# Optimization experiments

Measured on AMD Instinct MI355X. Metric: run time of the kernel, lower is better.

Reference implementation:

```python
import jax, jax.numpy as jnp
import numpy as np

EPS = 1e-5
C = 128
B = 16384
SYMBIOTIC = 4.0
NUM_PARENTS = 16
CHILDREN_PER_PARENT = 7


def _inverse(v):
    # torch: sort -> rank -> reversed rank -> gather sorted values
    idx0 = np.argsort(v, kind='stable')
    value = v[idx0]
    idx1 = np.argsort(idx0, kind='stable')  # ranks
    idx2 = v.shape[0] - 1 - idx1
    return value[idx2]


def _build_stats():
    counts = np.floor(50000.0 * 0.97 ** np.arange(C)) + 1.0  # long-tailed
    N = counts.sum()
    weight = (N / counts).astype(np.float32)
    prior = np.eye(C, dtype=np.float32)
    for p in range(NUM_PARENTS):
        ch = NUM_PARENTS + CHILDREN_PER_PARENT * p + np.arange(CHILDREN_PER_PARENT)
        prior[p, ch] = 1.0
    prior_me = (prior == 0).astype(np.float32)          # 1 - prior, keep only exact 1s
    prior_ms = prior - np.eye(C, dtype=np.float32)      # prior (0/1) minus eye
    v1_sig = np.log(N / counts - 1.0 + EPS).astype(np.float32)
    v2_sig = _inverse(v1_sig).astype(np.float32)
    v1_sm = np.log(counts / N + EPS).astype(np.float32)
    v2_sm = _inverse(v1_sm).astype(np.float32)
    return weight, prior_me, prior_ms, v1_sig, v2_sig, v1_sm, v2_sm


def setup_inputs() -> dict:
    key = jax.random.key(0)
    k1, k2 = jax.random.split(key)
    weight, prior_me, prior_ms, v1s, v2s, v1m, v2m = _build_stats()
    logits = 0.5 * jax.random.normal(k1, (12, B, C), dtype=jnp.float32)
    target = (jax.random.uniform(k2, (B, C)) < 0.1).astype(jnp.float32)
    return {
        'logits': logits, 'target': target,
        'weight': jnp.asarray(weight),
        'prior_me': jnp.asarray(prior_me), 'prior_ms': jnp.asarray(prior_ms),
        'v1_sigmoid': jnp.asarray(v1s), 'v2_sigmoid': jnp.asarray(v2s),
        'v1_softmax': jnp.asarray(v1m), 'v2_softmax': jnp.asarray(v2m),
    }


def reference(logits, target, weight, prior_me, prior_ms,
              v1_sigmoid, v2_sigmoid, v1_softmax, v2_softmax):
    zero = jnp.zeros_like(v1_sigmoid)
    # experts 0-5: sigmoid variants (long-tailed / balanced / inversed, twice)
    sig_shift = jnp.stack([zero, v1_sigmoid, v1_sigmoid - v2_sigmoid] * 2)  # [6,C]
    a_sig = jax.nn.sigmoid(logits[:6] - sig_shift[:, None, :])
    # experts 6-11: local-softmax variants
    sm_shift = jnp.stack([zero, v1_softmax, v1_softmax - v2_softmax] * 2)   # [6,C]
    e = jnp.exp(logits[6:] + sm_shift[:, None, :])                          # [6,B,C]
    denom = jnp.einsum('ebc,cd->ebd', e, prior_me) + e
    a_sm = e / (denom + EPS)
    acti = jnp.clip(jnp.concatenate([a_sig, a_sm], axis=0), EPS, 1.0 - EPS)  # [12,B,C]
    # weighted BCE per expert, summed
    bce = -weight * (target * jnp.log(acti) + (1.0 - target) * jnp.log(1.0 - acti))
    loss = jnp.sum(jnp.mean(bce, axis=(1, 2)))
    # symbiotic regularizer on experts 3,4,5,9,10,11
    row_sum = jnp.sum(prior_ms, axis=1)                 # [C]
    n_nz = jnp.sum(row_sum > 0).astype(acti.dtype)
    bsz = acti.shape[1]

    def symb(a):  # a: [B,C] activated logits
        def step(acc, xs):
            mask_row, parent = xs                       # [C], [B]
            term = jnp.log1p(jnp.exp(a - parent[:, None]))  # [B,C]
            rs = jnp.sum(mask_row)
            contrib = jnp.where(rs > 0, jnp.sum(term * mask_row) / (bsz * rs), 0.0)
            return acc + contrib, None
        total, _ = jax.lax.scan(step, jnp.float32(0.0), (prior_ms, a.T))
        return total / n_nz

    reg = jax.vmap(symb)(acti[jnp.array([3, 4, 5, 9, 10, 11])])
    return loss + SYMBIOTIC * jnp.sum(reg)
```

## Files before the change

### kernel.cpp

```cpp
#include <hip/hip_runtime.h>
#include <math.h>

#define CC 128
#define BB 16384
#define MEPS 1e-5f
#define NBLK 2048
#define PSZ ((size_t)BB * CC)


__device__ __forceinline__ float softplus1(float d) {
    const float u = d * d;
    float p = fmaf(u, 3.4722222e-4f, -5.2083333e-3f);
    p = fmaf(u, p, 0.125f);
    return fmaf(u, p, fmaf(d, 0.5f, 0.69314718f));
}

__global__ __launch_bounds__(256) void mel_main(
    const float* __restrict__ logits, const float* __restrict__ target,
    const float* __restrict__ weight,
    const float* __restrict__ v1s, const float* __restrict__ v2s,
    const float* __restrict__ v1m, const float* __restrict__ v2m,
    float* __restrict__ partial)
{
    const int lane = threadIdx.x & 63;
    const int wib  = threadIdx.x >> 6;
    const int wave = blockIdx.x * 4 + wib;
    const int r    = lane >> 5;
    const int c    = lane & 31;
    const size_t ro = (size_t)(wave * 2 + r) * CC;

    const float4 wt4 = ((const float4*)weight)[c];
    const float4 s1v = ((const float4*)v1s)[c];
    const float4 s2v = ((const float4*)v2s)[c];
    const float4 m1v = ((const float4*)v1m)[c];
    const float4 m2v = ((const float4*)v2m)[c];
    const float4 tv  = ((const float4*)(target + ro))[c];

    const float wt[4] = {wt4.x, wt4.y, wt4.z, wt4.w};
    const float s1[4] = {s1v.x, s1v.y, s1v.z, s1v.w};
    const float sd[4] = {s1v.x - s2v.x, s1v.y - s2v.y, s1v.z - s2v.z, s1v.w - s2v.w};
    const float m1[4] = {m1v.x, m1v.y, m1v.z, m1v.w};
    const float md[4] = {m1v.x - m2v.x, m1v.y - m2v.y, m1v.z - m2v.z, m1v.w - m2v.w};
    const bool  tb[4] = {tv.x > 0.5f, tv.y > 0.5f, tv.z > 0.5f, tv.w > 0.5f};

    const float childf = (c >= 4) ? 1.f : 0.f;
    int pofs[4];
    #pragma unroll
    for (int k = 0; k < 4; ++k) {
        const int ch = 4 * c + k;
        pofs[k] = (ch >= 16) ? (ch - 16) / 7 : 0;
    }

    __shared__ float lds[4][2][3][16];
    float* Lp = &lds[wib][r][0][0];

    const float* plane = logits + ro;
    float4 L0 = ((const float4*)plane)[c];
    float4 L1 = ((const float4*)(plane + PSZ))[c];
    float4 L2 = ((const float4*)(plane + 2 * PSZ))[c];
    plane += 3 * PSZ;

    float PnA[4] = {1.f, 1.f, 1.f, 1.f}, PdA[4] = {1.f, 1.f, 1.f, 1.f};
    float PnB[4] = {1.f, 1.f, 1.f, 1.f}, PdB[4] = {1.f, 1.f, 1.f, 1.f};
    float accS = 0.f;

    #pragma unroll 1
    for (int g = 0; g < 2; ++g) {
        const float x0[4] = {L0.x, L0.y, L0.z, L0.w};
        const float x1[4] = {L1.x, L1.y, L1.z, L1.w};
        const float x2[4] = {L2.x, L2.y, L2.z, L2.w};
        L0 = ((const float4*)plane)[c];
        L1 = ((const float4*)(plane + PSZ))[c];
        L2 = ((const float4*)(plane + 2 * PSZ))[c];
        plane += 3 * PSZ;

        float av[3][4];
        #pragma unroll
        for (int si = 0; si < 3; ++si) {
            #pragma unroll
            for (int k = 0; k < 4; ++k) {
                const float x  = (si == 0) ? x0[k] : (si == 1) ? x1[k] : x2[k];
                const float sh = (si == 0) ? 0.f   : (si == 1) ? s1[k] : sd[k];
                const float ex = __expf(sh - x);
                const float d  = 1.f + ex;
                PdA[k] *= d;
                PnA[k] *= tb[k] ? 1.f : ex;
                if (g == 1) av[si][k] = __builtin_amdgcn_rcpf(d);
            }
        }
        if (g == 1) {
            if (c < 4) {
                #pragma unroll
                for (int si = 0; si < 3; ++si)
                    *(float4*)(Lp + si * 16 + 4 * c) =
                        make_float4(av[si][0], av[si][1], av[si][2], av[si][3]);
            }
            #pragma unroll
            for (int si = 0; si < 3; ++si)
                #pragma unroll
                for (int k = 0; k < 4; ++k)
                    accS = fmaf(childf, softplus1(av[si][k] - Lp[si * 16 + pofs[k]]), accS);
        }
    }

    #pragma unroll 1
    for (int g = 0; g < 2; ++g) {
        const float x0[4] = {L0.x, L0.y, L0.z, L0.w};
        const float x1[4] = {L1.x, L1.y, L1.z, L1.w};
        const float x2[4] = {L2.x, L2.y, L2.z, L2.w};
        if (g == 0) {
            L0 = ((const float4*)plane)[c];
            L1 = ((const float4*)(plane + PSZ))[c];
            L2 = ((const float4*)(plane + 2 * PSZ))[c];
        }

        float ex[3][4], S[3];
        #pragma unroll
        for (int si = 0; si < 3; ++si) {
            S[si] = 0.f;
            #pragma unroll
            for (int k = 0; k < 4; ++k) {
                const float x  = (si == 0) ? x0[k] : (si == 1) ? x1[k] : x2[k];
                const float sh = (si == 0) ? 0.f   : (si == 1) ? m1[k] : md[k];
                ex[si][k] = __expf(x + sh);
                S[si] += ex[si][k];
            }
        }
        #pragma unroll
        for (int off = 16; off > 0; off >>= 1)
            #pragma unroll
            for (int si = 0; si < 3; ++si)
                S[si] += __shfl_xor(S[si], off, 64);

        if (c < 4) {
            #pragma unroll
            for (int si = 0; si < 3; ++si)
                *(float4*)(Lp + si * 16 + 4 * c) =
                    make_float4(ex[si][0], ex[si][1], ex[si][2], ex[si][3]);
        }

        #pragma unroll
        for (int si = 0; si < 3; ++si) {
            const float Sj = S[si] + MEPS;
            const float rS = __builtin_amdgcn_rcpf(Sj);
            #pragma unroll
            for (int k = 0; k < 4; ++k) {
                const float ep  = Lp[si * 16 + pofs[k]];
                const float den = Sj - childf * ep;
                const float e   = ex[si][k];
                const float ec  = fmaxf(e, MEPS * den);
                PnB[k] *= tb[k] ? ec : den - ec;
                PdB[k] *= den;
                if (g == 1) {
                    const float a  = ec * __builtin_amdgcn_rcpf(den);
                    const float ap = fmaxf(ep * rS, MEPS);
                    accS = fmaf(childf, softplus1(a - ap), accS);
                }
            }
        }
    }

    float accP = 0.f;
    #pragma unroll
    for (int k = 0; k < 4; ++k) {
        const float lg = (__logf(PdA[k]) - __logf(PnA[k]))
                       + (__logf(PdB[k]) - __logf(PnB[k]));
        accP = fmaf(wt[k], lg, accP);
    }

    float val = accP * (1.f / ((float)BB * (float)CC))
              + accS * (4.f / (112.f * (float)BB));

    #pragma unroll
    for (int off = 32; off > 0; off >>= 1)
        val += __shfl_xor(val, off, 64);

    __shared__ float sdata[4];
    if (lane == 0) sdata[wib] = val;
    __syncthreads();
    if (threadIdx.x == 0)
        partial[blockIdx.x] = (sdata[0] + sdata[1]) + (sdata[2] + sdata[3]);
}

__global__ __launch_bounds__(256) void mel_reduce(
    const float* __restrict__ partial, float* __restrict__ out)
{
    float v = 0.f;
    #pragma unroll
    for (int i = 0; i < NBLK / 256; ++i)
        v += partial[threadIdx.x + i * 256];
    #pragma unroll
    for (int off = 32; off > 0; off >>= 1)
        v += __shfl_xor(v, off, 64);
    __shared__ float s[4];
    const int lane = threadIdx.x & 63, wib = threadIdx.x >> 6;
    if (lane == 0) s[wib] = v;
    __syncthreads();
    if (threadIdx.x == 0) out[0] = (s[0] + s[1]) + (s[2] + s[3]);
}

extern "C" void kernel_launch(void* const* d_in, const int* in_sizes, int n_in,
                              void* d_out, int out_size, void* d_ws, size_t ws_size,
                              hipStream_t stream) {
    const float* logits = (const float*)d_in[0];
    const float* target = (const float*)d_in[1];
    const float* weight = (const float*)d_in[2];
    const float* v1s = (const float*)d_in[5];
    const float* v2s = (const float*)d_in[6];
    const float* v1m = (const float*)d_in[7];
    const float* v2m = (const float*)d_in[8];
    float* partial = (float*)d_ws;
    float* out = (float*)d_out;

    mel_main<<<NBLK, 256, 0, stream>>>(logits, target, weight,
                                       v1s, v2s, v1m, v2m, partial);
    mel_reduce<<<1, 256, 0, stream>>>(partial, out);
}
```

Before: 169.3 us.

## Replace sigmoid numerator product with logit sum and fuse final reduction via atomics

The sigmoid BCE numerator is no longer built as a running product of exponentials; it is rewritten algebraically as (1-t) times the sum of shifted logits, which avoids a product that can overflow or underflow. The logs switch to log2 scaled by ln2. The separate reduction kernel is replaced by a per-block atomicAdd into the output, preceded by a memset. This removes a second kernel launch at the cost of 2048 atomics on one address and a memset, and it makes the summation order nondeterministic.

```diff
diff --git a/kernel.cpp b/kernel.cpp
--- a/kernel.cpp
+++ b/kernel.cpp
@@ -6,6 +6,7 @@
 #define MEPS 1e-5f
 #define NBLK 2048
 #define PSZ ((size_t)BB * CC)
+#define LN2 0.6931471805599453f
 
 
 __device__ __forceinline__ float softplus1(float d) {
@@ -20,7 +21,7 @@
     const float* __restrict__ weight,
     const float* __restrict__ v1s, const float* __restrict__ v2s,
     const float* __restrict__ v1m, const float* __restrict__ v2m,
-    float* __restrict__ partial)
+    float* __restrict__ out)
 {
     const int lane = threadIdx.x & 63;
     const int wib  = threadIdx.x >> 6;
@@ -41,6 +42,7 @@
     const float sd[4] = {s1v.x - s2v.x, s1v.y - s2v.y, s1v.z - s2v.z, s1v.w - s2v.w};
     const float m1[4] = {m1v.x, m1v.y, m1v.z, m1v.w};
     const float md[4] = {m1v.x - m2v.x, m1v.y - m2v.y, m1v.z - m2v.z, m1v.w - m2v.w};
+    const float tn[4] = {1.f - tv.x, 1.f - tv.y, 1.f - tv.z, 1.f - tv.w};
     const bool  tb[4] = {tv.x > 0.5f, tv.y > 0.5f, tv.z > 0.5f, tv.w > 0.5f};
 
     const float childf = (c >= 4) ? 1.f : 0.f;
@@ -60,8 +62,9 @@
     float4 L2 = ((const float4*)(plane + 2 * PSZ))[c];
     plane += 3 * PSZ;
 
-    float PnA[4] = {1.f, 1.f, 1.f, 1.f}, PdA[4] = {1.f, 1.f, 1.f, 1.f};
-    float PnB[4] = {1.f, 1.f, 1.f, 1.f}, PdB[4] = {1.f, 1.f, 1.f, 1.f};
+    float PdA[4]  = {1.f, 1.f, 1.f, 1.f};
+    float PnB[4]  = {1.f, 1.f, 1.f, 1.f}, PdB[4] = {1.f, 1.f, 1.f, 1.f};
+    float zsum[4] = {0.f, 0.f, 0.f, 0.f};
     float accS = 0.f;
 
     #pragma unroll 1
@@ -84,7 +87,7 @@
                 const float ex = __expf(sh - x);
                 const float d  = 1.f + ex;
                 PdA[k] *= d;
-                PnA[k] *= tb[k] ? 1.f : ex;
+                zsum[k] += x - sh;
                 if (g == 1) av[si][k] = __builtin_amdgcn_rcpf(d);
             }
         }
@@ -163,9 +166,8 @@
     float accP = 0.f;
     #pragma unroll
     for (int k = 0; k < 4; ++k) {
-        const float lg = (__logf(PdA[k]) - __logf(PnA[k]))
-                       + (__logf(PdB[k]) - __logf(PnB[k]));
-        accP = fmaf(wt[k], lg, accP);
+        const float lg = LN2 * ((__log2f(PdA[k]) + __log2f(PdB[k])) - __log2f(PnB[k]));
+        accP = fmaf(wt[k], fmaf(tn[k], zsum[k], lg), accP);
     }
 
     float val = accP * (1.f / ((float)BB * (float)CC))
@@ -179,24 +181,7 @@
     if (lane == 0) sdata[wib] = val;
     __syncthreads();
     if (threadIdx.x == 0)
-        partial[blockIdx.x] = (sdata[0] + sdata[1]) + (sdata[2] + sdata[3]);
-}
-
-__global__ __launch_bounds__(256) void mel_reduce(
-    const float* __restrict__ partial, float* __restrict__ out)
-{
-    float v = 0.f;
-    #pragma unroll
-    for (int i = 0; i < NBLK / 256; ++i)
-        v += partial[threadIdx.x + i * 256];
-    #pragma unroll
-    for (int off = 32; off > 0; off >>= 1)
-        v += __shfl_xor(v, off, 64);
-    __shared__ float s[4];
-    const int lane = threadIdx.x & 63, wib = threadIdx.x >> 6;
-    if (lane == 0) s[wib] = v;
-    __syncthreads();
-    if (threadIdx.x == 0) out[0] = (s[0] + s[1]) + (s[2] + s[3]);
+        atomicAdd(out, (sdata[0] + sdata[1]) + (sdata[2] + sdata[3]));
 }
 
 extern "C" void kernel_launch(void* const* d_in, const int* in_sizes, int n_in,
@@ -209,10 +194,9 @@
     const float* v2s = (const float*)d_in[6];
     const float* v1m = (const float*)d_in[7];
     const float* v2m = (const float*)d_in[8];
-    float* partial = (float*)d_ws;
     float* out = (float*)d_out;
 
+    hipMemsetAsync(out, 0, sizeof(float), stream);
     mel_main<<<NBLK, 256, 0, stream>>>(logits, target, weight,
-                                       v1s, v2s, v1m, v2m, partial);
-    mel_reduce<<<1, 256, 0, stream>>>(partial, out);
+                                       v1s, v2s, v1m, v2m, out);
 }
```

Measured after the change: 172.4 us. Within noise of the previous version (+1.8%).
